# Performance work log

Measured on AMD Instinct MI355X. Metric: run time of the kernel, lower is better.

## Reference

```python
import jax, jax.numpy as jnp
import numpy as np

T, B, I, H, K = 200, 2048, 128, 128, 4


def setup_inputs() -> dict:
    key = jax.random.key(0)
    ks = jax.random.split(key, 7)
    inputs = jax.random.normal(ks[0], (T, B, I), jnp.float32)
    lengths = jax.random.randint(ks[1], (B,), 1, T + 1, jnp.int32)
    si = 1.0 / np.sqrt(I)
    sh = 1.0 / np.sqrt(H)
    w0 = jax.random.uniform(ks[2], (H,), jnp.float32, -sh, sh)      # Linear(H,1,bias=False)
    w1_w = jax.random.uniform(ks[3], (H, I), jnp.float32, -si, si)  # Linear(I,H)
    w1_b = jax.random.uniform(ks[4], (H,), jnp.float32, -si, si)
    w2_w = jax.random.uniform(ks[5], (H, I), jnp.float32, -si, si)  # Linear(I,H,bias=False)
    w3_w = jax.random.uniform(ks[6], (H, I), jnp.float32, -si, si)  # Linear(I,H,bias=False)
    return dict(inputs=inputs, lengths=lengths, label_len=4,
                w0=w0, w1_w=w1_w, w1_b=w1_b, w2_w=w2_w, w3_w=w3_w)


def reference(inputs, lengths, label_len, w0, w1_w, w1_b, w2_w, w3_w):
    # inputs: [T, B, I] time-major padded sequences; lengths: [B]
    T_, B_, _ = inputs.shape
    Kl = label_len
    dt = inputs.dtype
    # packed semantics: padded positions are exactly zero
    valid = (jnp.arange(T_)[:, None] < lengths[None, :])  # [T, B]
    x = inputs * valid[..., None].astype(dt)
    x1 = x @ w1_w.T + w1_b                                 # [T, B, H]
    x2 = x @ w2_w.T                                        # [T, B, H]
    # running mean m_s[t] = mean(inputs[:t+1]) (zeros at padding, as in torch)
    m_s = jnp.cumsum(x, axis=0) / jnp.arange(1, T_ + 1, dtype=dt)[:, None, None]
    # labeled timesteps: last min(L, label_len) steps of each sequence
    start = jnp.maximum(lengths - Kl, 0)                   # [B]
    t_lab = start[:, None] + jnp.arange(Kl)[None, :]       # [B, K]
    lab_valid = t_lab < lengths[:, None]                   # [B, K]
    t_c = jnp.minimum(t_lab, T_ - 1)
    b_idx = jnp.arange(B_)[:, None]
    x2_lab = x2[t_c, b_idx]                                # [B, K, H]
    wms_lab = m_s[t_c, b_idx] @ w3_w.T                     # [B, K, H]
    c = x2_lab + wms_lab                                   # [B, K, H]
    # att[b,k,s] = w0 . sigmoid(x1[s,b] + x2[t_k,b] + wms[t_k,b])
    att = jnp.einsum('sbkh,h->bks',
                     jax.nn.sigmoid(x1[:, :, None, :] + c[None, :, :, :]), w0)
    causal = (jnp.arange(T_)[None, None, :] <= t_lab[:, :, None]) & lab_valid[:, :, None]
    att = att * causal.astype(dt)                          # [B, K, T]
    h = jnp.einsum('bks,sbh->bkh', att, x1) + x2_lab       # [B, K, H]
    return h * lab_valid[..., None].astype(dt)
```

## Files before the change

### kernel.cpp

```cpp
#include <hip/hip_runtime.h>
#include <stdint.h>

#define T_DIM 200
#define B_DIM 2048
#define I_DIM 128
#define H_DIM 128
#define TS    32

typedef float  f32x4  __attribute__((ext_vector_type(4)));
typedef __bf16 bf16x8 __attribute__((ext_vector_type(8)));

union BF8 { ushort4 u2[2]; bf16x8 v; };

static __device__ __forceinline__ unsigned short f2bf(float f) {
    union { float f; unsigned u; } c; c.f = f;
    unsigned u = c.u + (0x7FFFu + ((c.u >> 16) & 1u));
    return (unsigned short)(u >> 16);
}
static __device__ __forceinline__ float bf2f(unsigned short s) {
    union { unsigned u; float f; } c; c.u = ((unsigned)s) << 16;
    return c.f;
}

__global__ __launch_bounds__(256, 4) void fused_kernel(
    const float* __restrict__ x, const int* __restrict__ lengths,
    const float* __restrict__ w0, const float* __restrict__ w1,
    const float* __restrict__ b1, const float* __restrict__ w2,
    const float* __restrict__ w3, float* __restrict__ out)
{
    __shared__ __align__(16) unsigned short xs[TS][136];
    __shared__ __align__(16) unsigned short x1s[TS][130];
    __shared__ __align__(16) float attp[TS][36];
    __shared__ __align__(16) float attk[TS][4];
    __shared__ __align__(16) float ektL[H_DIM][4];
    __shared__ __align__(16) float x2ls[4][H_DIM];
    __shared__ __align__(16) float w0s[H_DIM];
    __shared__ __align__(16) unsigned short axl[4][136];
    __shared__ __align__(16) unsigned short ams[4][136];

    const int b    = blockIdx.x;
    const int tid  = threadIdx.x;
    const int lane = tid & 63;
    const int wv   = tid >> 6;
    const int l15  = lane & 15;
    const int quad = lane >> 4;
    const int L     = lengths[b];
    const int start = (L > 4) ? (L - 4) : 0;
    const int nv    = (L < 4) ? L : 4;

    if (tid < 128) w0s[tid] = w0[tid];

    bf16x8 bfr[2][4];
    float  bias[2];
    #pragma unroll
    for (int nt = 0; nt < 2; ++nt) {
        const int n = wv * 32 + nt * 16 + l15;
        bias[nt] = b1[n];
        #pragma unroll
        for (int ks = 0; ks < 4; ++ks) {
            const int kc = ks * 32 + quad * 8;
            const float4 p0 = *(const float4*)(w1 + (size_t)n * I_DIM + kc);
            const float4 p1 = *(const float4*)(w1 + (size_t)n * I_DIM + kc + 4);
            BF8 t;
            t.u2[0] = make_ushort4(f2bf(p0.x), f2bf(p0.y), f2bf(p0.z), f2bf(p0.w));
            t.u2[1] = make_ushort4(f2bf(p1.x), f2bf(p1.y), f2bf(p1.z), f2bf(p1.w));
            bfr[nt][ks] = t.v;
        }
    }

    const int i    = tid & 127;
    const int half = tid >> 7;
    const int m    = start >> 1;
    const float* xp = x + (size_t)b * I_DIM + i;
    {
        const int tb = half ? m : 0;
        const int te = half ? start : m;
        float s = 0.f;
        int t = tb;
        for (; t + 4 <= te; t += 4) {
            const float a0 = xp[(size_t)(t + 0) * (B_DIM * I_DIM)];
            const float a1 = xp[(size_t)(t + 1) * (B_DIM * I_DIM)];
            const float a2 = xp[(size_t)(t + 2) * (B_DIM * I_DIM)];
            const float a3 = xp[(size_t)(t + 3) * (B_DIM * I_DIM)];
            s += a0 + a1 + a2 + a3;
        }
        for (; t < te; ++t) s += xp[(size_t)t * (B_DIM * I_DIM)];
        float* psum = &attp[0][0];
        psum[half * 128 + i] = s;
    }
    __syncthreads();

    if (tid < 128) {
        float* psum = &attp[0][0];
        float p = psum[i] + psum[128 + i];
        const float v0 = xp[(size_t)(start + 0) * (B_DIM * I_DIM)];
        const float v1 = xp[(size_t)(start + 1) * (B_DIM * I_DIM)];
        const float v2 = xp[(size_t)(start + 2) * (B_DIM * I_DIM)];
        const float v3 = xp[(size_t)(start + 3) * (B_DIM * I_DIM)];
        const float p0 = p + v0, p1 = p0 + v1, p2 = p1 + v2, p3 = p2 + v3;
        axl[0][i] = f2bf(v0); axl[1][i] = f2bf(v1);
        axl[2][i] = f2bf(v2); axl[3][i] = f2bf(v3);
        ams[0][i] = f2bf(p0 / (float)(start + 1));
        ams[1][i] = f2bf(p1 / (float)(start + 2));
        ams[2][i] = f2bf(p2 / (float)(start + 3));
        ams[3][i] = f2bf(p3 / (float)(start + 4));
    }
    __syncthreads();

    #pragma unroll
    for (int nt = 0; nt < 2; ++nt) {
        const int n = wv * 32 + nt * 16 + l15;
        f32x4 c1 = (f32x4){0.f, 0.f, 0.f, 0.f};
        f32x4 c2 = (f32x4){0.f, 0.f, 0.f, 0.f};
        #pragma unroll
        for (int ks = 0; ks < 4; ++ks) {
            const int kc = ks * 32 + quad * 8;
            const bf16x8 a1 = *(const bf16x8*)&axl[l15 & 3][kc];
            const bf16x8 a2 = *(const bf16x8*)&ams[l15 & 3][kc];
            const float4 q0 = *(const float4*)(w2 + (size_t)n * I_DIM + kc);
            const float4 q1 = *(const float4*)(w2 + (size_t)n * I_DIM + kc + 4);
            const float4 r0 = *(const float4*)(w3 + (size_t)n * I_DIM + kc);
            const float4 r1 = *(const float4*)(w3 + (size_t)n * I_DIM + kc + 4);
            BF8 bw2, bw3;
            bw2.u2[0] = make_ushort4(f2bf(q0.x), f2bf(q0.y), f2bf(q0.z), f2bf(q0.w));
            bw2.u2[1] = make_ushort4(f2bf(q1.x), f2bf(q1.y), f2bf(q1.z), f2bf(q1.w));
            bw3.u2[0] = make_ushort4(f2bf(r0.x), f2bf(r0.y), f2bf(r0.z), f2bf(r0.w));
            bw3.u2[1] = make_ushort4(f2bf(r1.x), f2bf(r1.y), f2bf(r1.z), f2bf(r1.w));
            c1 = __builtin_amdgcn_mfma_f32_16x16x32_bf16(a1, bw2.v, c1, 0, 0, 0);
            c2 = __builtin_amdgcn_mfma_f32_16x16x32_bf16(a2, bw3.v, c2, 0, 0, 0);
        }
        if (quad == 0) {
            #pragma unroll
            for (int r = 0; r < 4; ++r) {
                x2ls[r][n] = c1[r];
                ektL[n][r] = __builtin_amdgcn_exp2f(-1.44269504f * (c1[r] + c2[r]));
            }
        }
    }
    __syncthreads();

    const int sq = tid & 31;
    const int hg = tid >> 5;
    const int hcol = tid & 127;
    float hacc0 = 0.f, hacc1 = 0.f, hacc2v = 0.f, hacc3 = 0.f;

    for (int t0 = 0; t0 < L; t0 += TS) {
        const int nrows = (L - t0 < TS) ? (L - t0) : TS;

        #pragma unroll
        for (int it = 0; it < 4; ++it) {
            const int sl = tid + it * 256;
            const int r = sl >> 5, f4 = sl & 31;
            ushort4 w = make_ushort4(0, 0, 0, 0);
            if (r < nrows) {
                const float4 v = *(const float4*)(
                    x + ((size_t)(t0 + r) * B_DIM + b) * I_DIM + f4 * 4);
                w = make_ushort4(f2bf(v.x), f2bf(v.y), f2bf(v.z), f2bf(v.w));
            }
            *(ushort4*)&xs[r][f4 * 4] = w;
        }
        __syncthreads();

        #pragma unroll
        for (int mt = 0; mt < 2; ++mt) {
            bf16x8 afr[4];
            #pragma unroll
            for (int ks = 0; ks < 4; ++ks)
                afr[ks] = *(const bf16x8*)&xs[mt * 16 + l15][ks * 32 + quad * 8];
            #pragma unroll
            for (int nt = 0; nt < 2; ++nt) {
                f32x4 acc = (f32x4){0.f, 0.f, 0.f, 0.f};
                #pragma unroll
                for (int ks = 0; ks < 4; ++ks)
                    acc = __builtin_amdgcn_mfma_f32_16x16x32_bf16(
                        afr[ks], bfr[nt][ks], acc, 0, 0, 0);
                const int h = wv * 32 + nt * 16 + l15;
                const int tr = mt * 16 + quad * 4;
                #pragma unroll
                for (int r = 0; r < 4; ++r)
                    x1s[tr + r][h] = f2bf(acc[r] + bias[nt]);
            }
        }
        __syncthreads();

        {
            const int h0 = hg * 16;
            f32x4 a = (f32x4){0.f, 0.f, 0.f, 0.f};
            #pragma unroll
            for (int hh = 0; hh < 16; hh += 2) {
                const int h = h0 + hh;
                const unsigned xv2 = *(const unsigned*)&x1s[sq][h];
                const float xa = bf2f((unsigned short)(xv2 & 0xFFFFu));
                const float xb = bf2f((unsigned short)(xv2 >> 16));
                const float Ea = __builtin_amdgcn_exp2f(-1.44269504f * xa);
                const float Eb = __builtin_amdgcn_exp2f(-1.44269504f * xb);
                const f32x4 eka = *(const f32x4*)&ektL[h][0];
                const f32x4 ekb = *(const f32x4*)&ektL[h + 1][0];
                const float wa = w0s[h], wb = w0s[h + 1];
                #pragma unroll
                for (int k = 0; k < 4; ++k)
                    a[k] += wa * __builtin_amdgcn_rcpf(1.f + Ea * eka[k])
                          + wb * __builtin_amdgcn_rcpf(1.f + Eb * ekb[k]);
            }
            *(f32x4*)&attp[sq][hg * 4] = a;
        }
        __syncthreads();

        if (tid < TS) {
            const int s = t0 + tid;
            f32x4 sm = (f32x4){0.f, 0.f, 0.f, 0.f};
            #pragma unroll
            for (int g = 0; g < 8; ++g)
                sm += *(const f32x4*)&attp[tid][g * 4];
            f32x4 o;
            o[0] = (0 < nv && s <= start    ) ? sm[0] : 0.f;
            o[1] = (1 < nv && s <= start + 1) ? sm[1] : 0.f;
            o[2] = (2 < nv && s <= start + 2) ? sm[2] : 0.f;
            o[3] = (3 < nv && s <= start + 3) ? sm[3] : 0.f;
            *(f32x4*)&attk[tid][0] = o;
        }
        __syncthreads();

        {
            const int sbase = half * 16;
            #pragma unroll
            for (int s2 = 0; s2 < 16; ++s2) {
                const int srow = sbase + s2;
                const f32x4 a4 = *(const f32x4*)&attk[srow][0];
                const float xv = bf2f(x1s[srow][hcol]);
                hacc0 += a4[0] * xv; hacc1 += a4[1] * xv;
                hacc2v += a4[2] * xv; hacc3 += a4[3] * xv;
            }
        }
        __syncthreads();
    }

    {
        float* h2 = &attp[0][0];
        if (half == 1) {
            *(f32x4*)&h2[hcol * 4] = (f32x4){hacc0, hacc1, hacc2v, hacc3};
        }
        __syncthreads();
        if (tid < 128) {
            const f32x4 o = *(const f32x4*)&h2[hcol * 4];
            hacc0 += o[0]; hacc1 += o[1]; hacc2v += o[2]; hacc3 += o[3];
            out[((size_t)b * 4 + 0) * H_DIM + hcol] = (0 < nv) ? hacc0 + x2ls[0][hcol] : 0.f;
            out[((size_t)b * 4 + 1) * H_DIM + hcol] = (1 < nv) ? hacc1 + x2ls[1][hcol] : 0.f;
            out[((size_t)b * 4 + 2) * H_DIM + hcol] = (2 < nv) ? hacc2v + x2ls[2][hcol] : 0.f;
            out[((size_t)b * 4 + 3) * H_DIM + hcol] = (3 < nv) ? hacc3 + x2ls[3][hcol] : 0.f;
        }
    }
}

extern "C" void kernel_launch(void* const* d_in, const int* in_sizes, int n_in,
                              void* d_out, int out_size, void* d_ws, size_t ws_size,
                              hipStream_t stream) {
    (void)in_sizes; (void)n_in; (void)out_size; (void)d_ws; (void)ws_size;
    const float* x       = (const float*)d_in[0];
    const int*   lengths = (const int*)d_in[1];
    const float* w0 = (const float*)d_in[3];
    const float* w1 = (const float*)d_in[4];
    const float* b1 = (const float*)d_in[5];
    const float* w2 = (const float*)d_in[6];
    const float* w3 = (const float*)d_in[7];
    float* out = (float*)d_out;

    fused_kernel<<<dim3(B_DIM), 256, 0, stream>>>(x, lengths, w0, w1, b1, w2, w3, out);
}
```

Measured before the change: 386.8 us.

## Prefetch next input tile into registers and coalesce prefix-sum loads

New measurement: 402.0 us. 3.9% more time.

```diff
diff --git a/kernel.cpp b/kernel.cpp
--- a/kernel.cpp
+++ b/kernel.cpp
@@ -13,13 +13,15 @@
 union BF8 { ushort4 u2[2]; bf16x8 v; };
 
 static __device__ __forceinline__ unsigned short f2bf(float f) {
-    union { float f; unsigned u; } c; c.f = f;
-    unsigned u = c.u + (0x7FFFu + ((c.u >> 16) & 1u));
-    return (unsigned short)(u >> 16);
+    union { __bf16 b; unsigned short u; } c; c.b = (__bf16)f;
+    return c.u;
 }
 static __device__ __forceinline__ float bf2f(unsigned short s) {
     union { unsigned u; float f; } c; c.u = ((unsigned)s) << 16;
     return c.f;
+}
+static __device__ __forceinline__ ushort4 cvt4(float4 v) {
+    return make_ushort4(f2bf(v.x), f2bf(v.y), f2bf(v.z), f2bf(v.w));
 }
 
 __global__ __launch_bounds__(256, 4) void fused_kernel(
@@ -50,6 +52,28 @@
 
     if (tid < 128) w0s[tid] = w0[tid];
 
+    const int sr0 = tid >> 5;
+    const int sf4 = tid & 31;
+
+    float4 stg[4];
+    #pragma unroll
+    for (int it = 0; it < 4; ++it) {
+        const int t = it * 8 + sr0;
+        stg[it] = make_float4(0.f, 0.f, 0.f, 0.f);
+        if (t < L)
+            stg[it] = *(const float4*)(x + ((size_t)t * B_DIM + b) * I_DIM + sf4 * 4);
+    }
+
+    const int i = tid & 127;
+    const float* xp = x + (size_t)b * I_DIM + i;
+    float v0 = 0.f, v1 = 0.f, v2 = 0.f, v3 = 0.f;
+    if (tid < 128) {
+        v0 = xp[(size_t)(start + 0) * (B_DIM * I_DIM)];
+        v1 = xp[(size_t)(start + 1) * (B_DIM * I_DIM)];
+        v2 = xp[(size_t)(start + 2) * (B_DIM * I_DIM)];
+        v3 = xp[(size_t)(start + 3) * (B_DIM * I_DIM)];
+    }
+
     bf16x8 bfr[2][4];
     float  bias[2];
     #pragma unroll
@@ -62,41 +86,37 @@
             const float4 p0 = *(const float4*)(w1 + (size_t)n * I_DIM + kc);
             const float4 p1 = *(const float4*)(w1 + (size_t)n * I_DIM + kc + 4);
             BF8 t;
-            t.u2[0] = make_ushort4(f2bf(p0.x), f2bf(p0.y), f2bf(p0.z), f2bf(p0.w));
-            t.u2[1] = make_ushort4(f2bf(p1.x), f2bf(p1.y), f2bf(p1.z), f2bf(p1.w));
+            t.u2[0] = cvt4(p0);
+            t.u2[1] = cvt4(p1);
             bfr[nt][ks] = t.v;
         }
     }
 
-    const int i    = tid & 127;
-    const int half = tid >> 7;
-    const int m    = start >> 1;
-    const float* xp = x + (size_t)b * I_DIM + i;
     {
-        const int tb = half ? m : 0;
-        const int te = half ? start : m;
-        float s = 0.f;
-        int t = tb;
-        for (; t + 4 <= te; t += 4) {
-            const float a0 = xp[(size_t)(t + 0) * (B_DIM * I_DIM)];
-            const float a1 = xp[(size_t)(t + 1) * (B_DIM * I_DIM)];
-            const float a2 = xp[(size_t)(t + 2) * (B_DIM * I_DIM)];
-            const float a3 = xp[(size_t)(t + 3) * (B_DIM * I_DIM)];
-            s += a0 + a1 + a2 + a3;
-        }
-        for (; t < te; ++t) s += xp[(size_t)t * (B_DIM * I_DIM)];
+        const float* xq = x + (size_t)b * I_DIM + sf4 * 4;
+        const size_t RS = (size_t)B_DIM * I_DIM;
+        f32x4 s0 = (f32x4){0.f, 0.f, 0.f, 0.f};
+        f32x4 s1 = s0, s2 = s0, s3 = s0;
+        int t = sr0;
+        for (; t + 24 < start; t += 32) {
+            s0 += *(const f32x4*)(xq + (size_t)(t     ) * RS);
+            s1 += *(const f32x4*)(xq + (size_t)(t +  8) * RS);
+            s2 += *(const f32x4*)(xq + (size_t)(t + 16) * RS);
+            s3 += *(const f32x4*)(xq + (size_t)(t + 24) * RS);
+        }
+        for (; t < start; t += 8)
+            s0 += *(const f32x4*)(xq + (size_t)t * RS);
+        const f32x4 s = (s0 + s1) + (s2 + s3);
         float* psum = &attp[0][0];
-        psum[half * 128 + i] = s;
+        *(f32x4*)&psum[sr0 * 132 + sf4 * 4] = s;
     }
     __syncthreads();
 
     if (tid < 128) {
-        float* psum = &attp[0][0];
-        float p = psum[i] + psum[128 + i];
-        const float v0 = xp[(size_t)(start + 0) * (B_DIM * I_DIM)];
-        const float v1 = xp[(size_t)(start + 1) * (B_DIM * I_DIM)];
-        const float v2 = xp[(size_t)(start + 2) * (B_DIM * I_DIM)];
-        const float v3 = xp[(size_t)(start + 3) * (B_DIM * I_DIM)];
+        const float* psum = &attp[0][0];
+        float p = 0.f;
+        #pragma unroll
+        for (int g = 0; g < 8; ++g) p += psum[g * 132 + i];
         const float p0 = p + v0, p1 = p0 + v1, p2 = p1 + v2, p3 = p2 + v3;
         axl[0][i] = f2bf(v0); axl[1][i] = f2bf(v1);
         axl[2][i] = f2bf(v2); axl[3][i] = f2bf(v3);
@@ -122,10 +142,8 @@
             const float4 r0 = *(const float4*)(w3 + (size_t)n * I_DIM + kc);
             const float4 r1 = *(const float4*)(w3 + (size_t)n * I_DIM + kc + 4);
             BF8 bw2, bw3;
-            bw2.u2[0] = make_ushort4(f2bf(q0.x), f2bf(q0.y), f2bf(q0.z), f2bf(q0.w));
-            bw2.u2[1] = make_ushort4(f2bf(q1.x), f2bf(q1.y), f2bf(q1.z), f2bf(q1.w));
-            bw3.u2[0] = make_ushort4(f2bf(r0.x), f2bf(r0.y), f2bf(r0.z), f2bf(r0.w));
-            bw3.u2[1] = make_ushort4(f2bf(r1.x), f2bf(r1.y), f2bf(r1.z), f2bf(r1.w));
+            bw2.u2[0] = cvt4(q0); bw2.u2[1] = cvt4(q1);
+            bw3.u2[0] = cvt4(r0); bw3.u2[1] = cvt4(r1);
             c1 = __builtin_amdgcn_mfma_f32_16x16x32_bf16(a1, bw2.v, c1, 0, 0, 0);
             c2 = __builtin_amdgcn_mfma_f32_16x16x32_bf16(a2, bw3.v, c2, 0, 0, 0);
         }
@@ -142,24 +160,26 @@
     const int sq = tid & 31;
     const int hg = tid >> 5;
     const int hcol = tid & 127;
+    const int half = tid >> 7;
     float hacc0 = 0.f, hacc1 = 0.f, hacc2v = 0.f, hacc3 = 0.f;
 
     for (int t0 = 0; t0 < L; t0 += TS) {
-        const int nrows = (L - t0 < TS) ? (L - t0) : TS;
-
-        #pragma unroll
-        for (int it = 0; it < 4; ++it) {
-            const int sl = tid + it * 256;
-            const int r = sl >> 5, f4 = sl & 31;
-            ushort4 w = make_ushort4(0, 0, 0, 0);
-            if (r < nrows) {
-                const float4 v = *(const float4*)(
-                    x + ((size_t)(t0 + r) * B_DIM + b) * I_DIM + f4 * 4);
-                w = make_ushort4(f2bf(v.x), f2bf(v.y), f2bf(v.z), f2bf(v.w));
-            }
-            *(ushort4*)&xs[r][f4 * 4] = w;
-        }
-        __syncthreads();
+        #pragma unroll
+        for (int it = 0; it < 4; ++it)
+            *(ushort4*)&xs[it * 8 + sr0][sf4 * 4] = cvt4(stg[it]);
+        __syncthreads();
+
+        {
+            const int tn = t0 + TS;
+            #pragma unroll
+            for (int it = 0; it < 4; ++it) {
+                const int t = tn + it * 8 + sr0;
+                stg[it] = make_float4(0.f, 0.f, 0.f, 0.f);
+                if (t < L)
+                    stg[it] = *(const float4*)(
+                        x + ((size_t)t * B_DIM + b) * I_DIM + sf4 * 4);
+            }
+        }
 
         #pragma unroll
         for (int mt = 0; mt < 2; ++mt) {
@@ -202,7 +222,11 @@
                     a[k] += wa * __builtin_amdgcn_rcpf(1.f + Ea * eka[k])
                           + wb * __builtin_amdgcn_rcpf(1.f + Eb * ekb[k]);
             }
-            *(f32x4*)&attp[sq][hg * 4] = a;
+            #pragma unroll
+            for (int k = 0; k < 4; ++k)
+                a[k] += __shfl_xor(a[k], 32);
+            if (!(tid & 32))
+                *(f32x4*)&attp[sq][(tid >> 6) * 4] = a;
         }
         __syncthreads();
 
@@ -210,7 +234,7 @@
             const int s = t0 + tid;
             f32x4 sm = (f32x4){0.f, 0.f, 0.f, 0.f};
             #pragma unroll
-            for (int g = 0; g < 8; ++g)
+            for (int g = 0; g < 4; ++g)
                 sm += *(const f32x4*)&attp[tid][g * 4];
             f32x4 o;
             o[0] = (0 < nv && s <= start    ) ? sm[0] : 0.f;
```
